# Optimization experiments

Hardware: AMD Instinct MI355X
Metric: run time of the kernel (lower is better)

Reference implementation:

```python
import jax, jax.numpy as jnp
import numpy as np

C = 256; NH = 8; HD = C // NH; NL = 4; NP = 4; DFF = 1024
B = 8; NQ = 900
SHAPES = ((100, 100), (50, 50), (25, 25), (13, 13))
LEN = sum(h * w for h, w in SHAPES)


def setup_inputs() -> dict:
    key = jax.random.key(0)
    ks = jax.random.split(key, 16)
    s = 0.02
    d = {}
    d['tgt'] = jax.random.normal(ks[0], (B, NQ, C), jnp.float32)
    d['query_pos'] = jax.random.normal(ks[1], (B, NQ, C), jnp.float32)
    d['reference_points'] = jax.random.uniform(ks[2], (B, NQ, NL, 2), jnp.float32)
    d['src'] = jax.random.normal(ks[3], (B, LEN, C), jnp.float32)
    d['spatial_shapes'] = np.array(SHAPES, dtype=np.int32)
    # self-attn (nn.MultiheadAttention) params, stored [in,out]
    d['sa_in_w'] = jax.random.normal(ks[4], (C, 3 * C), jnp.float32) * s
    d['sa_in_b'] = jnp.zeros((3 * C,), jnp.float32)
    d['sa_out_w'] = jax.random.normal(ks[5], (C, C), jnp.float32) * s
    d['sa_out_b'] = jnp.zeros((C,), jnp.float32)
    d['ln2_g'] = jnp.ones((C,), jnp.float32); d['ln2_b'] = jnp.zeros((C,), jnp.float32)
    # MSDeformAttn params
    d['off_w'] = jax.random.normal(ks[6], (C, NH * NL * NP * 2), jnp.float32) * s
    d['off_b'] = jax.random.normal(ks[7], (NH * NL * NP * 2,), jnp.float32) * 0.5
    d['attw_w'] = jax.random.normal(ks[8], (C, NH * NL * NP), jnp.float32) * s
    d['attw_b'] = jnp.zeros((NH * NL * NP,), jnp.float32)
    d['val_w'] = jax.random.normal(ks[9], (C, C), jnp.float32) * s
    d['val_b'] = jnp.zeros((C,), jnp.float32)
    d['proj_w'] = jax.random.normal(ks[10], (C, C), jnp.float32) * s
    d['proj_b'] = jnp.zeros((C,), jnp.float32)
    d['ln1_g'] = jnp.ones((C,), jnp.float32); d['ln1_b'] = jnp.zeros((C,), jnp.float32)
    # FFN
    d['lin1_w'] = jax.random.normal(ks[11], (C, DFF), jnp.float32) * s
    d['lin1_b'] = jnp.zeros((DFF,), jnp.float32)
    d['lin2_w'] = jax.random.normal(ks[12], (DFF, C), jnp.float32) * s
    d['lin2_b'] = jnp.zeros((C,), jnp.float32)
    d['ln3_g'] = jnp.ones((C,), jnp.float32); d['ln3_b'] = jnp.zeros((C,), jnp.float32)
    return d


def _ln(x, g, b):
    m = jnp.mean(x, -1, keepdims=True)
    v = jnp.mean((x - m) ** 2, -1, keepdims=True)
    return (x - m) * jax.lax.rsqrt(v + 1e-5) * g + b


def _bilinear(v, loc, H, W):
    # v: [B,NH,H*W,HD]; loc: [B,NQ,NH,NP,2] normalized to [0,1]
    # matches F.grid_sample(align_corners=False, padding_mode='zeros')
    b = v.shape[0]; nq = loc.shape[1]
    x = loc[..., 0] * W - 0.5
    y = loc[..., 1] * H - 0.5
    x0 = jnp.floor(x); y0 = jnp.floor(y)
    dx = x - x0; dy = y - y0
    x0i = x0.astype(jnp.int32); y0i = y0.astype(jnp.int32)

    def gat(ix, iy):
        valid = ((ix >= 0) & (ix < W) & (iy >= 0) & (iy < H)).astype(v.dtype)
        idx = jnp.clip(iy, 0, H - 1) * W + jnp.clip(ix, 0, W - 1)  # [B,NQ,NH,NP]
        idx_t = jnp.transpose(idx, (0, 2, 1, 3)).reshape(b, NH, nq * NP)
        g = jnp.take_along_axis(v, idx_t[..., None], axis=2).reshape(b, NH, nq, NP, HD)
        return g * jnp.transpose(valid, (0, 2, 1, 3))[..., None]

    wt = lambda a: jnp.transpose(a, (0, 2, 1, 3))[..., None]
    return (gat(x0i, y0i) * wt((1 - dx) * (1 - dy))
            + gat(x0i + 1, y0i) * wt(dx * (1 - dy))
            + gat(x0i, y0i + 1) * wt((1 - dx) * dy)
            + gat(x0i + 1, y0i + 1) * wt(dx * dy))


def _msda(q, ref, src, shapes, val_w, val_b, off_w, off_b, attw_w, attw_b, proj_w, proj_b):
    b, nq, _ = q.shape
    value = jnp.transpose((src @ val_w + val_b).reshape(b, -1, NH, HD), (0, 2, 1, 3))  # [B,NH,Len,HD]
    off = (q @ off_w + off_b).reshape(b, nq, NH, NL, NP, 2)
    aw = jax.nn.softmax((q @ attw_w + attw_b).reshape(b, nq, NH, NL * NP), -1)
    aw = aw.reshape(b, nq, NH, NL, NP)
    acc = jnp.zeros((b, NH, nq, HD), q.dtype)
    start = 0
    for l, (H_, W_) in enumerate(shapes):
        norm = jnp.array([W_, H_], q.dtype)
        loc = ref[:, :, None, l, None, :] + off[:, :, :, l] / norm  # [B,NQ,NH,NP,2]
        smp = _bilinear(value[:, :, start:start + H_ * W_], loc, H_, W_)  # [B,NH,NQ,NP,HD]
        acc = acc + jnp.sum(smp * jnp.transpose(aw[:, :, :, l], (0, 2, 1, 3))[..., None], axis=3)
        start += H_ * W_
    out = jnp.transpose(acc, (0, 2, 1, 3)).reshape(b, nq, C)
    return out @ proj_w + proj_b


def _self_attn(x, pos, in_w, in_b, out_w, out_b):
    b, nq, _ = x.shape
    qk = x + pos
    q = (qk @ in_w[:, :C] + in_b[:C]).reshape(b, nq, NH, HD)
    k = (qk @ in_w[:, C:2 * C] + in_b[C:2 * C]).reshape(b, nq, NH, HD)
    v = (x @ in_w[:, 2 * C:] + in_b[2 * C:]).reshape(b, nq, NH, HD)
    att = jax.nn.softmax(jnp.einsum('bqhd,bkhd->bhqk', q, k) * (1.0 / float(np.sqrt(HD))), -1)
    o = jnp.einsum('bhqk,bkhd->bqhd', att, v).reshape(b, nq, C)
    return o @ out_w + out_b


def _forward(tgt, query_pos, reference_points, src, shapes,
             sa_in_w, sa_in_b, sa_out_w, sa_out_b, ln2_g, ln2_b,
             off_w, off_b, attw_w, attw_b, val_w, val_b, proj_w, proj_b, ln1_g, ln1_b,
             lin1_w, lin1_b, lin2_w, lin2_b, ln3_g, ln3_b):
    t2 = _self_attn(tgt, query_pos, sa_in_w, sa_in_b, sa_out_w, sa_out_b)
    t = _ln(tgt + t2, ln2_g, ln2_b)
    t2 = _msda(t + query_pos, reference_points, src, shapes,
               val_w, val_b, off_w, off_b, attw_w, attw_b, proj_w, proj_b)
    t = _ln(t + t2, ln1_g, ln1_b)
    h = jax.nn.relu(t @ lin1_w + lin1_b) @ lin2_w + lin2_b
    return _ln(t + h, ln3_g, ln3_b)


def reference(tgt, query_pos, reference_points, src, spatial_shapes,
              sa_in_w, sa_in_b, sa_out_w, sa_out_b, ln2_g, ln2_b,
              off_w, off_b, attw_w, attw_b, val_w, val_b, proj_w, proj_b, ln1_g, ln1_b,
              lin1_w, lin1_b, lin2_w, lin2_b, ln3_g, ln3_b):
    shapes = [(int(h), int(w)) for h, w in np.asarray(spatial_shapes)]
    return _forward(tgt, query_pos, reference_points, src, shapes,
                    sa_in_w, sa_in_b, sa_out_w, sa_out_b, ln2_g, ln2_b,
                    off_w, off_b, attw_w, attw_b, val_w, val_b, proj_w, proj_b, ln1_g, ln1_b,
                    lin1_w, lin1_b, lin2_w, lin2_b, ln3_g, ln3_b)
```

## Files before the change

### kernel.cpp

```cpp
#include <hip/hip_runtime.h>
#include <hip/hip_bf16.h>
#include <type_traits>

#define C_DIM 256
#define NHEAD 8
#define HDIM 32
#define NLVL 4
#define NPT 4
#define DFF_DIM 1024
#define BB 8
#define NQ_DIM 900
#define LEN_DIM 13294
#define ROWS (BB * NQ_DIM)
#define VROWS (BB * LEN_DIM)

typedef __attribute__((ext_vector_type(8))) short short8v;
typedef __attribute__((ext_vector_type(8))) unsigned short ushort8v;
typedef __attribute__((ext_vector_type(4))) float float4v;
typedef __attribute__((ext_vector_type(4))) unsigned short ushort4v;

__device__ __forceinline__ float bf2f(unsigned short u) {
  union { unsigned int i; float f; } v; v.i = ((unsigned int)u) << 16; return v.f;
}
__device__ __forceinline__ unsigned short f2bf(float f) {
  __hip_bfloat16 h = __float2bfloat16(f);
  return *reinterpret_cast<unsigned short*>(&h);
}

__global__ __launch_bounds__(256) void wconv_kernel(
    const float* __restrict__ w0, const float* __restrict__ w1,
    const float* __restrict__ w2, const float* __restrict__ w3,
    const float* __restrict__ w4, const float* __restrict__ w5,
    const float* __restrict__ w6, const float* __restrict__ w7,
    unsigned short* __restrict__ out) {
  const int Ks[8] = {256, 256, 256, 256, 256, 256, 256, 1024};
  const int Ns[8] = {768, 256, 256, 128, 256, 256, 1024, 256};
  const int Oo[8] = {0, 196608, 262144, 327680, 360448, 425984, 491520, 753664};
  int w = blockIdx.y;
  int K = Ks[w], N = Ns[w];
  int ntx = N >> 5, nty = K >> 5;
  if ((int)blockIdx.x >= ntx * nty) return;
  int tx = blockIdx.x % ntx, ty = blockIdx.x / ntx;
  const float* W = w == 0 ? w0 : w == 1 ? w1 : w == 2 ? w2 : w == 3 ? w3
                 : w == 4 ? w4 : w == 5 ? w5 : w == 6 ? w6 : w7;
  __shared__ float tile[32][33];
  int c = threadIdx.x & 31, rg = threadIdx.x >> 5;
#pragma unroll
  for (int j = 0; j < 4; ++j) {
    int k = ty * 32 + rg * 4 + j;
    tile[rg * 4 + j][c] = W[(size_t)k * N + tx * 32 + c];
  }
  __syncthreads();
  unsigned short* o = out + Oo[w];
#pragma unroll
  for (int j = 0; j < 4; ++j) {
    int n = tx * 32 + rg * 4 + j;
    o[(size_t)n * K + ty * 32 + c] = f2bf(tile[c][rg * 4 + j]);
  }
}

__global__ __launch_bounds__(256) void prep_kernel(const float* __restrict__ a,
                                                   const float* __restrict__ b,
                                                   unsigned short* __restrict__ o1,
                                                   unsigned short* __restrict__ o2, int n4) {
  int i = blockIdx.x * 256 + threadIdx.x;
  if (i < n4) {
    float4 x = reinterpret_cast<const float4*>(a)[i];
    float4 y = reinterpret_cast<const float4*>(b)[i];
    ushort4v u1, u2;
    u1[0] = f2bf(x.x); u1[1] = f2bf(x.y); u1[2] = f2bf(x.z); u1[3] = f2bf(x.w);
    u2[0] = f2bf(x.x + y.x); u2[1] = f2bf(x.y + y.y);
    u2[2] = f2bf(x.z + y.z); u2[3] = f2bf(x.w + y.w);
    *reinterpret_cast<ushort4v*>(o1 + (size_t)i * 4) = u1;
    *reinterpret_cast<ushort4v*>(o2 + (size_t)i * 4) = u2;
  }
}

template <typename TA, typename TO, int RELU>
__device__ __forceinline__ void gemm_body(
    unsigned short* smem,
    const TA* __restrict__ A, const TA* __restrict__ A2,
    const unsigned short* __restrict__ Wt,
    const float* __restrict__ bias, const float* __restrict__ bias2,
    TO* __restrict__ Cout, TO* __restrict__ Cout2,
    int M, int N, int K, int lda, int ldc, int ldc2, int colSplit,
    int bx, int by) {
  auto Al = reinterpret_cast<unsigned short(*)[128][40]>(smem);
  auto Wl = reinterpret_cast<unsigned short(*)[128][40]>(smem + 10240);
  const int tid = threadIdx.x;
  const int lane = tid & 63, wid = tid >> 6;
  const int g = lane >> 4, ql = lane & 15;
  const int wr = wid >> 1, wc = wid & 1;
  const int row0 = by * 128, col0 = bx * 128;

  const TA* Ause = (A2 != nullptr && col0 >= colSplit) ? A2 : A;

  float4v acc[4][4];
#pragma unroll
  for (int i = 0; i < 4; ++i)
#pragma unroll
    for (int j = 0; j < 4; ++j) acc[i][j] = (float4v){0.f, 0.f, 0.f, 0.f};

  float4 areg_f[4];
  ushort8v areg_b[2];
  ushort8v wreg[2];

  auto loadA = [&](int k0) {
    if constexpr (std::is_same<TA, float>::value) {
#pragma unroll
      for (int j = 0; j < 4; ++j) {
        int c = tid + 256 * j;
        int row = c >> 3, f4 = c & 7;
        int gr = min(row0 + row, M - 1);
        areg_f[j] = *reinterpret_cast<const float4*>(Ause + (size_t)gr * lda + k0 + f4 * 4);
      }
    } else {
#pragma unroll
      for (int j = 0; j < 2; ++j) {
        int c = tid + 256 * j;
        int row = c >> 2, ch = c & 3;
        int gr = min(row0 + row, M - 1);
        areg_b[j] = *reinterpret_cast<const ushort8v*>(
            reinterpret_cast<const unsigned short*>(Ause) + (size_t)gr * lda + k0 + ch * 8);
      }
    }
  };
  auto loadW = [&](int k0) {
#pragma unroll
    for (int j = 0; j < 2; ++j) {
      int c = tid + 256 * j;
      int row = c >> 2, ch = c & 3;
      wreg[j] = *reinterpret_cast<const ushort8v*>(
          Wt + (size_t)(col0 + row) * K + k0 + ch * 8);
    }
  };
  auto storeA = [&](int buf) {
    if constexpr (std::is_same<TA, float>::value) {
#pragma unroll
      for (int j = 0; j < 4; ++j) {
        int c = tid + 256 * j;
        int row = c >> 3, f4 = c & 7;
        ushort4v u;
        u[0] = f2bf(areg_f[j].x); u[1] = f2bf(areg_f[j].y);
        u[2] = f2bf(areg_f[j].z); u[3] = f2bf(areg_f[j].w);
        *reinterpret_cast<ushort4v*>(&Al[buf][row][f4 * 4]) = u;
      }
    } else {
#pragma unroll
      for (int j = 0; j < 2; ++j) {
        int c = tid + 256 * j;
        int row = c >> 2, ch = c & 3;
        *reinterpret_cast<ushort8v*>(&Al[buf][row][ch * 8]) = areg_b[j];
      }
    }
  };
  auto storeW = [&](int buf) {
#pragma unroll
    for (int j = 0; j < 2; ++j) {
      int c = tid + 256 * j;
      int row = c >> 2, ch = c & 3;
      *reinterpret_cast<ushort8v*>(&Wl[buf][row][ch * 8]) = wreg[j];
    }
  };

  const int nt = K >> 5;
  loadA(0); loadW(0);
  storeA(0); storeW(0);

  for (int t = 0; t < nt; ++t) {
    __syncthreads();
    if (t + 1 < nt) { loadA((t + 1) << 5); loadW((t + 1) << 5); }
    const int cur = t & 1;
    short8v af[4], bfr[4];
#pragma unroll
    for (int mi = 0; mi < 4; ++mi)
      af[mi] = *reinterpret_cast<const short8v*>(&Al[cur][wr * 64 + mi * 16 + ql][8 * g]);
#pragma unroll
    for (int ni = 0; ni < 4; ++ni)
      bfr[ni] = *reinterpret_cast<const short8v*>(&Wl[cur][wc * 64 + ni * 16 + ql][8 * g]);
#pragma unroll
    for (int mi = 0; mi < 4; ++mi)
#pragma unroll
      for (int ni = 0; ni < 4; ++ni)
        acc[mi][ni] = __builtin_amdgcn_mfma_f32_16x16x32_bf16(af[mi], bfr[ni], acc[mi][ni], 0, 0, 0);
    if (t + 1 < nt) { storeA(cur ^ 1); storeW(cur ^ 1); }
  }

  const bool sel2 = (Cout2 != nullptr && col0 >= colSplit);
  const float* bsrc = sel2 ? bias2 : bias;
  TO* outp = sel2 ? Cout2 : Cout;
  const int ldco = sel2 ? ldc2 : ldc;
  const int cbase = sel2 ? (col0 - colSplit) : col0;
  float bv[4];
#pragma unroll
  for (int ni = 0; ni < 4; ++ni) bv[ni] = bsrc[cbase + wc * 64 + ni * 16 + ql];
#pragma unroll
  for (int mi = 0; mi < 4; ++mi) {
#pragma unroll
    for (int r = 0; r < 4; ++r) {
      int row = row0 + wr * 64 + mi * 16 + 4 * g + r;
      if (row >= M) continue;
#pragma unroll
      for (int ni = 0; ni < 4; ++ni) {
        int col = cbase + wc * 64 + ni * 16 + ql;
        float v = acc[mi][ni][r] + bv[ni];
        if (RELU) v = fmaxf(v, 0.f);
        if constexpr (std::is_same<TO, float>::value) {
          outp[(size_t)row * ldco + col] = v;
        } else {
          outp[(size_t)row * ldco + col] = __float2bfloat16(v);
        }
      }
    }
  }
}

template <typename TA, typename TO, int RELU>
__global__ __launch_bounds__(256) void mfma_gemm_kernel(
    const TA* __restrict__ A, const TA* __restrict__ A2,
    const unsigned short* __restrict__ Wt,
    const float* __restrict__ bias, const float* __restrict__ bias2,
    TO* __restrict__ Cout, TO* __restrict__ Cout2,
    int M, int N, int K, int lda, int ldc, int ldc2, int colSplit) {
  __shared__ unsigned short smem[20480];
  gemm_body<TA, TO, RELU>(smem, A, A2, Wt, bias, bias2, Cout, Cout2,
                          M, N, K, lda, ldc, ldc2, colSplit,
                          blockIdx.x, blockIdx.y);
}

#define QKV_BLOCKS (6 * 57)
__global__ __launch_bounds__(256) void qkv_value_kernel(
    const unsigned short* __restrict__ x0bf, const unsigned short* __restrict__ tgtbf,
    const unsigned short* __restrict__ sa_inT, const float* __restrict__ sa_in_b,
    __hip_bfloat16* __restrict__ qkv,
    const float* __restrict__ src, const unsigned short* __restrict__ valT,
    const float* __restrict__ val_b, __hip_bfloat16* __restrict__ value) {
  __shared__ unsigned short smem[20480];
  int bid = blockIdx.x;
  if (bid < QKV_BLOCKS) {
    gemm_body<unsigned short, __hip_bfloat16, 0>(
        smem, x0bf, tgtbf, sa_inT, sa_in_b, nullptr, qkv, nullptr,
        ROWS, 768, 256, 256, 768, 0, 512, bid % 6, bid / 6);
  } else {
    int t = bid - QKV_BLOCKS;
    gemm_body<float, __hip_bfloat16, 0>(
        smem, src, nullptr, valT, val_b, nullptr, value, nullptr,
        VROWS, 256, 256, 256, 256, 0, 1 << 30, t & 1, t >> 1);
  }
}

__global__ __launch_bounds__(256) void ln_fused_kernel(const float* __restrict__ x,
                                                       const float* __restrict__ y,
                                                       const float* __restrict__ gg,
                                                       const float* __restrict__ bb,
                                                       float* __restrict__ out,
                                                       unsigned short* __restrict__ out2,
                                                       const float* __restrict__ qadd) {
  int row = blockIdx.x, t = threadIdx.x;
  size_t base = (size_t)row * C_DIM + t;
  float v = x[base] + y[base];
  float s = v, s2 = v * v;
#pragma unroll
  for (int o = 32; o > 0; o >>= 1) {
    s += __shfl_xor(s, o);
    s2 += __shfl_xor(s2, o);
  }
  __shared__ float w1[4], w2[4];
  int wid = t >> 6, lane = t & 63;
  if (lane == 0) { w1[wid] = s; w2[wid] = s2; }
  __syncthreads();
  float S = w1[0] + w1[1] + w1[2] + w1[3];
  float S2 = w2[0] + w2[1] + w2[2] + w2[3];
  float mean = S * (1.f / 256.f);
  float var = S2 * (1.f / 256.f) - mean * mean;
  float rstd = rsqrtf(var + 1e-5f);
  float r = (v - mean) * rstd * gg[t] + bb[t];
  out[base] = r;
  if (out2) {
    float r2 = qadd ? (r + qadd[base]) : r;
    out2[base] = f2bf(r2);
  }
}

__global__ __launch_bounds__(256) void self_attn_mfma_kernel(
    const unsigned short* __restrict__ qkv, unsigned short* __restrict__ out) {
  __shared__ unsigned short V_lds[2][32][16];
  __shared__ unsigned short P_lds[4][16][32];
  const int tid = threadIdx.x;
  const int lane = tid & 63, wid = tid >> 6;
  const int g = lane >> 4, ql = lane & 15;
  const int bh = blockIdx.y;
  const int b = bh >> 3, h = bh & 7;
  const int q0 = blockIdx.x * 64 + wid * 16;
  const float scale = 0.17677669529663687f;

  const unsigned short* qkv_b = qkv + (size_t)b * NQ_DIM * 768;
  const int qrow = min(q0 + ql, NQ_DIM - 1);
  short8v qf = *reinterpret_cast<const short8v*>(
      qkv_b + (size_t)qrow * 768 + h * HDIM + 8 * g);

  float4v o0 = {0.f, 0.f, 0.f, 0.f}, o1 = {0.f, 0.f, 0.f, 0.f};
  float m = -1e30f, lsum = 0.f;

  const int sk = tid >> 3;
  const int sd = (tid & 7) * 4;
  const int sdb = sd >> 4, sdi = sd & 15;

  const int NT = 29;
  for (int kt = 0; kt < NT; ++kt) {
    __syncthreads();
    {
      int kg = min(kt * 32 + sk, NQ_DIM - 1);
      ushort4v v4 = *reinterpret_cast<const ushort4v*>(
          qkv_b + (size_t)kg * 768 + 512 + h * HDIM + sd);
      *reinterpret_cast<ushort4v*>(&V_lds[sdb][sk][sdi]) = v4;
    }
    __syncthreads();

    const int k_base = kt * 32;
    int kr0 = min(k_base + ql, NQ_DIM - 1);
    int kr1 = min(k_base + 16 + ql, NQ_DIM - 1);
    short8v kf0 = *reinterpret_cast<const short8v*>(
        qkv_b + (size_t)kr0 * 768 + 256 + h * HDIM + 8 * g);
    short8v kf1 = *reinterpret_cast<const short8v*>(
        qkv_b + (size_t)kr1 * 768 + 256 + h * HDIM + 8 * g);
    float4v z = {0.f, 0.f, 0.f, 0.f};
    float4v s0 = __builtin_amdgcn_mfma_f32_16x16x32_bf16(kf0, qf, z, 0, 0, 0);
    float4v s1 = __builtin_amdgcn_mfma_f32_16x16x32_bf16(kf1, qf, z, 0, 0, 0);

    float s[8];
#pragma unroll
    for (int r = 0; r < 4; ++r) { s[r] = s0[r] * scale; s[4 + r] = s1[r] * scale; }
    if (kt == NT - 1) {
#pragma unroll
      for (int i = 0; i < 8; ++i) {
        int kk = k_base + 16 * (i >> 2) + 4 * g + (i & 3);
        if (kk >= NQ_DIM) s[i] = -1e30f;
      }
    }
    float tm = s[0];
#pragma unroll
    for (int i = 1; i < 8; ++i) tm = fmaxf(tm, s[i]);
    tm = fmaxf(tm, __shfl_xor(tm, 16));
    tm = fmaxf(tm, __shfl_xor(tm, 32));
    float mnew = fmaxf(m, tm);
    float alpha = __expf(m - mnew);
    float p[8];
    float ts = 0.f;
#pragma unroll
    for (int i = 0; i < 8; ++i) { p[i] = __expf(s[i] - mnew); ts += p[i]; }
    ts += __shfl_xor(ts, 16);
    ts += __shfl_xor(ts, 32);
    lsum = lsum * alpha + ts;
    m = mnew;

    ushort4v pp0, pp1;
#pragma unroll
    for (int r = 0; r < 4; ++r) { pp0[r] = f2bf(p[r]); pp1[r] = f2bf(p[4 + r]); }
    *reinterpret_cast<ushort4v*>(&P_lds[wid][ql][4 * g]) = pp0;
    *reinterpret_cast<ushort4v*>(&P_lds[wid][ql][16 + 4 * g]) = pp1;
    asm volatile("s_waitcnt lgkmcnt(0)" ::: "memory");
    __builtin_amdgcn_sched_barrier(0);

    o0 *= alpha;
    o1 *= alpha;

    short8v pf = *reinterpret_cast<const short8v*>(&P_lds[wid][ql][8 * g]);
    short8v vf0, vf1;
#pragma unroll
    for (int i = 0; i < 8; ++i) {
      vf0[i] = (short)V_lds[0][8 * g + i][ql];
      vf1[i] = (short)V_lds[1][8 * g + i][ql];
    }
    o0 = __builtin_amdgcn_mfma_f32_16x16x32_bf16(vf0, pf, o0, 0, 0, 0);
    o1 = __builtin_amdgcn_mfma_f32_16x16x32_bf16(vf1, pf, o1, 0, 0, 0);
  }

  float inv = 1.f / lsum;
  if (q0 + ql < NQ_DIM) {
    unsigned short* op = out + ((size_t)(b * NQ_DIM) + q0 + ql) * C_DIM + h * HDIM;
    ushort4v u0, u1;
#pragma unroll
    for (int r = 0; r < 4; ++r) { u0[r] = f2bf(o0[r] * inv); u1[r] = f2bf(o1[r] * inv); }
    *reinterpret_cast<ushort4v*>(op + 4 * g) = u0;
    *reinterpret_cast<ushort4v*>(op + 16 + 4 * g) = u1;
  }
}

__global__ __launch_bounds__(256) void softmax16_kernel(float* __restrict__ aw, int total) {
  int t = blockIdx.x * 256 + threadIdx.x;
  if (t >= total) return;
  float* p = aw + (size_t)t * 16;
  float vals[16];
  float m = -1e30f;
#pragma unroll
  for (int i = 0; i < 16; ++i) { vals[i] = p[i]; m = fmaxf(m, vals[i]); }
  float s = 0.f;
#pragma unroll
  for (int i = 0; i < 16; ++i) { vals[i] = __expf(vals[i] - m); s += vals[i]; }
  float inv = 1.f / s;
#pragma unroll
  for (int i = 0; i < 16; ++i) p[i] = vals[i] * inv;
}

__global__ __launch_bounds__(256) void msda_sample_kernel(
    const unsigned short* __restrict__ value,
    const float* __restrict__ off,
    const float* __restrict__ aw,
    const float* __restrict__ refp,
    const int* __restrict__ shapes,
    unsigned short* __restrict__ out) {
  int g = blockIdx.x * 32 + (threadIdx.x >> 3);
  int d4 = threadIdx.x & 7;
  int h = g & 7;
  int row = g >> 3;
  int b = row / NQ_DIM;
  float acc0 = 0.f, acc1 = 0.f, acc2 = 0.f, acc3 = 0.f;
  int start = 0;
  const float* offr = off + (size_t)row * 256 + h * 32;
  const float* awr  = aw + (size_t)row * 128 + h * 16;
  const float* rpr  = refp + (size_t)row * NLVL * 2;
#pragma unroll
  for (int l = 0; l < NLVL; ++l) {
    int Hl = shapes[2 * l], Wl = shapes[2 * l + 1];
    float fx = rpr[2 * l + 0] * (float)Wl - 0.5f;
    float fy = rpr[2 * l + 1] * (float)Hl - 0.5f;
    const unsigned short* vbase =
        value + ((size_t)(b * LEN_DIM + start)) * C_DIM + h * HDIM + d4 * 4;
#pragma unroll
    for (int p = 0; p < NPT; ++p) {
      float x = fx + offr[l * 8 + p * 2];
      float y = fy + offr[l * 8 + p * 2 + 1];
      float a = awr[l * 4 + p];
      float x0f = floorf(x), y0f = floorf(y);
      float dx = x - x0f, dy = y - y0f;
      int x0 = (int)x0f, y0 = (int)y0f;
      int x1 = x0 + 1, y1 = y0 + 1;
      float wx1 = dx, wx0 = 1.f - dx;
      float wy1 = dy * a, wy0 = (1.f - dy) * a;
      bool vx0 = ((unsigned)x0 < (unsigned)Wl);
      bool vx1 = ((unsigned)x1 < (unsigned)Wl);
      bool vy0 = ((unsigned)y0 < (unsigned)Hl);
      bool vy1 = ((unsigned)y1 < (unsigned)Hl);
      float w00 = (vx0 && vy0) ? wx0 * wy0 : 0.f;
      float w10 = (vx1 && vy0) ? wx1 * wy0 : 0.f;
      float w01 = (vx0 && vy1) ? wx0 * wy1 : 0.f;
      float w11 = (vx1 && vy1) ? wx1 * wy1 : 0.f;
      int x0c = min(max(x0, 0), Wl - 1), x1c = min(max(x1, 0), Wl - 1);
      int y0c = min(max(y0, 0), Hl - 1), y1c = min(max(y1, 0), Hl - 1);
      int r0 = y0c * Wl, r1 = y1c * Wl;
      ushort4v g00 = *reinterpret_cast<const ushort4v*>(vbase + ((r0 + x0c) << 8));
      ushort4v g10 = *reinterpret_cast<const ushort4v*>(vbase + ((r0 + x1c) << 8));
      ushort4v g01 = *reinterpret_cast<const ushort4v*>(vbase + ((r1 + x0c) << 8));
      ushort4v g11 = *reinterpret_cast<const ushort4v*>(vbase + ((r1 + x1c) << 8));
      acc0 += w00 * bf2f(g00[0]) + w10 * bf2f(g10[0]) + w01 * bf2f(g01[0]) + w11 * bf2f(g11[0]);
      acc1 += w00 * bf2f(g00[1]) + w10 * bf2f(g10[1]) + w01 * bf2f(g01[1]) + w11 * bf2f(g11[1]);
      acc2 += w00 * bf2f(g00[2]) + w10 * bf2f(g10[2]) + w01 * bf2f(g01[2]) + w11 * bf2f(g11[2]);
      acc3 += w00 * bf2f(g00[3]) + w10 * bf2f(g10[3]) + w01 * bf2f(g01[3]) + w11 * bf2f(g11[3]);
    }
    start += Hl * Wl;
  }
  ushort4v o;
  o[0] = f2bf(acc0); o[1] = f2bf(acc1); o[2] = f2bf(acc2); o[3] = f2bf(acc3);
  *reinterpret_cast<ushort4v*>(out + (size_t)row * C_DIM + h * HDIM + d4 * 4) = o;
}

extern "C" void kernel_launch(void* const* d_in, const int* in_sizes, int n_in,
                              void* d_out, int out_size, void* d_ws, size_t ws_size,
                              hipStream_t stream) {
  const float* tgt      = (const float*)d_in[0];
  const float* qpos     = (const float*)d_in[1];
  const float* refp     = (const float*)d_in[2];
  const float* src      = (const float*)d_in[3];
  const int*   shapes   = (const int*)d_in[4];
  const float* sa_in_w  = (const float*)d_in[5];
  const float* sa_in_b  = (const float*)d_in[6];
  const float* sa_out_w = (const float*)d_in[7];
  const float* sa_out_b = (const float*)d_in[8];
  const float* ln2_g    = (const float*)d_in[9];
  const float* ln2_b    = (const float*)d_in[10];
  const float* off_w    = (const float*)d_in[11];
  const float* off_b    = (const float*)d_in[12];
  const float* attw_w   = (const float*)d_in[13];
  const float* attw_b   = (const float*)d_in[14];
  const float* val_w    = (const float*)d_in[15];
  const float* val_b    = (const float*)d_in[16];
  const float* proj_w   = (const float*)d_in[17];
  const float* proj_b   = (const float*)d_in[18];
  const float* ln1_g    = (const float*)d_in[19];
  const float* ln1_b    = (const float*)d_in[20];
  const float* lin1_w   = (const float*)d_in[21];
  const float* lin1_b   = (const float*)d_in[22];
  const float* lin2_w   = (const float*)d_in[23];
  const float* lin2_b   = (const float*)d_in[24];
  const float* ln3_g    = (const float*)d_in[25];
  const float* ln3_b    = (const float*)d_in[26];

  char* ws = (char*)d_ws;
  size_t off_b_ws = 0;
  auto alloc = [&](size_t bytes) {
    char* p = ws + off_b_ws;
    off_b_ws += (bytes + 255) & ~(size_t)255;
    return p;
  };
  unsigned short* wT     = (unsigned short*)alloc((size_t)1015808 * 2);
  unsigned short* value  = (unsigned short*)alloc((size_t)VROWS * C_DIM * 2);
  unsigned short* qkvh   = (unsigned short*)alloc((size_t)ROWS * 768 * 2);
  unsigned short* tgtbf  = (unsigned short*)alloc((size_t)ROWS * C_DIM * 2);
  unsigned short* X0bf   = (unsigned short*)alloc((size_t)ROWS * C_DIM * 2);
  unsigned short* attnbf = (unsigned short*)alloc((size_t)ROWS * C_DIM * 2);
  unsigned short* X3bf   = (unsigned short*)alloc((size_t)ROWS * C_DIM * 2);
  unsigned short* sampbf = (unsigned short*)alloc((size_t)ROWS * C_DIM * 2);
  unsigned short* X6bf   = (unsigned short*)alloc((size_t)ROWS * C_DIM * 2);
  unsigned short* hidbf  = (unsigned short*)alloc((size_t)ROWS * DFF_DIM * 2);
  float* X1 = (float*)alloc((size_t)ROWS * C_DIM * 4);
  float* X2 = (float*)alloc((size_t)ROWS * C_DIM * 4);
  float* X4 = (float*)alloc((size_t)ROWS * C_DIM * 4);
  float* X5 = (float*)alloc((size_t)ROWS * 128 * 4);
  float* X6 = (float*)alloc((size_t)ROWS * C_DIM * 4);
  if (off_b_ws > ws_size) return;

  unsigned short* sa_inT = wT + 0;
  unsigned short* sa_outT = wT + 196608;
  unsigned short* offT   = wT + 262144;
  unsigned short* valT   = wT + 360448;
  unsigned short* projT  = wT + 425984;
  unsigned short* lin1T  = wT + 491520;
  unsigned short* lin2T  = wT + 753664;

  dim3 blk(256);
  const int MB7200 = (ROWS + 127) / 128;
  const int MBV = (VROWS + 127) / 128;
  int n4 = ROWS * C_DIM / 4;
  int addBlocks = (n4 + 255) / 256;

  wconv_kernel<<<dim3(256, 8), blk, 0, stream>>>(
      sa_in_w, sa_out_w, off_w, attw_w, val_w, proj_w, lin1_w, lin2_w, wT);
  prep_kernel<<<addBlocks, blk, 0, stream>>>(tgt, qpos, tgtbf, X0bf, n4);

  qkv_value_kernel<<<QKV_BLOCKS + 2 * MBV, blk, 0, stream>>>(
      X0bf, tgtbf, sa_inT, sa_in_b, (__hip_bfloat16*)qkvh,
      src, valT, val_b, (__hip_bfloat16*)value);

  self_attn_mfma_kernel<<<dim3(15, 64), blk, 0, stream>>>(qkvh, attnbf);
  mfma_gemm_kernel<unsigned short, float, 0><<<dim3(2, MB7200), blk, 0, stream>>>(
      attnbf, nullptr, sa_outT, sa_out_b, nullptr,
      X1, nullptr, ROWS, 256, 256, 256, 256, 0, 1 << 30);
  ln_fused_kernel<<<ROWS, blk, 0, stream>>>(tgt, X1, ln2_g, ln2_b, X2, X3bf, qpos);

  mfma_gemm_kernel<unsigned short, float, 0><<<dim3(3, MB7200), blk, 0, stream>>>(
      X3bf, nullptr, offT, off_b, attw_b,
      X4, X5, ROWS, 384, 256, 256, 256, 128, 256);
  softmax16_kernel<<<(ROWS * NHEAD + 255) / 256, blk, 0, stream>>>(X5, ROWS * NHEAD);
  msda_sample_kernel<<<ROWS * NHEAD / 32, blk, 0, stream>>>(
      value, X4, X5, refp, shapes, sampbf);
  mfma_gemm_kernel<unsigned short, float, 0><<<dim3(2, MB7200), blk, 0, stream>>>(
      sampbf, nullptr, projT, proj_b, nullptr,
      X1, nullptr, ROWS, 256, 256, 256, 256, 0, 1 << 30);
  ln_fused_kernel<<<ROWS, blk, 0, stream>>>(X2, X1, ln1_g, ln1_b, X6, X6bf, nullptr);

  mfma_gemm_kernel<unsigned short, __hip_bfloat16, 1><<<dim3(8, MB7200), blk, 0, stream>>>(
      X6bf, nullptr, lin1T, lin1_b, nullptr,
      (__hip_bfloat16*)hidbf, nullptr, ROWS, 1024, 256, 256, 1024, 0, 1 << 30);
  mfma_gemm_kernel<unsigned short, float, 0><<<dim3(2, MB7200), blk, 0, stream>>>(
      hidbf, nullptr, lin2T, lin2_b, nullptr,
      X1, nullptr, ROWS, 256, 1024, 1024, 256, 0, 1 << 30);
  ln_fused_kernel<<<ROWS, blk, 0, stream>>>(X6, X1, ln3_g, ln3_b, (float*)d_out, nullptr, nullptr);
}
```

Baseline: 230.8 us.

## Write V transposed from QKV GEMM epilogue and drop LDS V staging in self-attention

The QKV projection epilogue now writes Q and K to a 512-wide buffer and V to a per-batch transposed [C][928] buffer. The self-attention kernel can then load V fragments straight from global memory as contiguous short8 vectors. This removes the per-tile LDS staging, the scalar transpose gather and two __syncthreads per key tile. The weight-conversion and input-prep kernels are also merged into one launch to save launch overhead. In exchange, the transposed epilogue uses strided 2-byte global stores. The padded key columns 900..927 of the V buffer are never written, so garbage there (for example NaN) could leak into the output even though those keys get zero probability.

Measured after the change: 231.9 us. About the same (+0.5%).

```diff
diff --git a/kernel.cpp b/kernel.cpp
--- a/kernel.cpp
+++ b/kernel.cpp
@@ -13,6 +13,7 @@
 #define LEN_DIM 13294
 #define ROWS (BB * NQ_DIM)
 #define VROWS (BB * LEN_DIM)
+#define VT_LD 928
 
 typedef __attribute__((ext_vector_type(8))) short short8v;
 typedef __attribute__((ext_vector_type(8))) unsigned short ushort8v;
@@ -27,56 +28,57 @@
   return *reinterpret_cast<unsigned short*>(&h);
 }
 
-__global__ __launch_bounds__(256) void wconv_kernel(
+#define WCONV_BLOCKS 2048
+__global__ __launch_bounds__(256) void wprep_kernel(
     const float* __restrict__ w0, const float* __restrict__ w1,
     const float* __restrict__ w2, const float* __restrict__ w3,
     const float* __restrict__ w4, const float* __restrict__ w5,
     const float* __restrict__ w6, const float* __restrict__ w7,
-    unsigned short* __restrict__ out) {
-  const int Ks[8] = {256, 256, 256, 256, 256, 256, 256, 1024};
-  const int Ns[8] = {768, 256, 256, 128, 256, 256, 1024, 256};
-  const int Oo[8] = {0, 196608, 262144, 327680, 360448, 425984, 491520, 753664};
-  int w = blockIdx.y;
-  int K = Ks[w], N = Ns[w];
-  int ntx = N >> 5, nty = K >> 5;
-  if ((int)blockIdx.x >= ntx * nty) return;
-  int tx = blockIdx.x % ntx, ty = blockIdx.x / ntx;
-  const float* W = w == 0 ? w0 : w == 1 ? w1 : w == 2 ? w2 : w == 3 ? w3
-                 : w == 4 ? w4 : w == 5 ? w5 : w == 6 ? w6 : w7;
-  __shared__ float tile[32][33];
-  int c = threadIdx.x & 31, rg = threadIdx.x >> 5;
-#pragma unroll
-  for (int j = 0; j < 4; ++j) {
-    int k = ty * 32 + rg * 4 + j;
-    tile[rg * 4 + j][c] = W[(size_t)k * N + tx * 32 + c];
-  }
-  __syncthreads();
-  unsigned short* o = out + Oo[w];
-#pragma unroll
-  for (int j = 0; j < 4; ++j) {
-    int n = tx * 32 + rg * 4 + j;
-    o[(size_t)n * K + ty * 32 + c] = f2bf(tile[c][rg * 4 + j]);
-  }
-}
-
-__global__ __launch_bounds__(256) void prep_kernel(const float* __restrict__ a,
-                                                   const float* __restrict__ b,
-                                                   unsigned short* __restrict__ o1,
-                                                   unsigned short* __restrict__ o2, int n4) {
-  int i = blockIdx.x * 256 + threadIdx.x;
-  if (i < n4) {
-    float4 x = reinterpret_cast<const float4*>(a)[i];
-    float4 y = reinterpret_cast<const float4*>(b)[i];
-    ushort4v u1, u2;
-    u1[0] = f2bf(x.x); u1[1] = f2bf(x.y); u1[2] = f2bf(x.z); u1[3] = f2bf(x.w);
-    u2[0] = f2bf(x.x + y.x); u2[1] = f2bf(x.y + y.y);
-    u2[2] = f2bf(x.z + y.z); u2[3] = f2bf(x.w + y.w);
-    *reinterpret_cast<ushort4v*>(o1 + (size_t)i * 4) = u1;
-    *reinterpret_cast<ushort4v*>(o2 + (size_t)i * 4) = u2;
-  }
-}
-
-template <typename TA, typename TO, int RELU>
+    unsigned short* __restrict__ out,
+    const float* __restrict__ tgt, const float* __restrict__ qpos,
+    unsigned short* __restrict__ tgtbf, unsigned short* __restrict__ x0bf, int n4) {
+  int bid = blockIdx.x;
+  if (bid < WCONV_BLOCKS) {
+    const int Ks[8] = {256, 256, 256, 256, 256, 256, 256, 1024};
+    const int Ns[8] = {768, 256, 256, 128, 256, 256, 1024, 256};
+    const int Oo[8] = {0, 196608, 262144, 327680, 360448, 425984, 491520, 753664};
+    int w = bid >> 8, bx = bid & 255;
+    int K = Ks[w], N = Ns[w];
+    int ntx = N >> 5, nty = K >> 5;
+    if (bx >= ntx * nty) return;
+    int tx = bx % ntx, ty = bx / ntx;
+    const float* W = w == 0 ? w0 : w == 1 ? w1 : w == 2 ? w2 : w == 3 ? w3
+                   : w == 4 ? w4 : w == 5 ? w5 : w == 6 ? w6 : w7;
+    __shared__ float tile[32][33];
+    int c = threadIdx.x & 31, rg = threadIdx.x >> 5;
+#pragma unroll
+    for (int j = 0; j < 4; ++j) {
+      int k = ty * 32 + rg * 4 + j;
+      tile[rg * 4 + j][c] = W[(size_t)k * N + tx * 32 + c];
+    }
+    __syncthreads();
+    unsigned short* o = out + Oo[w];
+#pragma unroll
+    for (int j = 0; j < 4; ++j) {
+      int n = tx * 32 + rg * 4 + j;
+      o[(size_t)n * K + ty * 32 + c] = f2bf(tile[c][rg * 4 + j]);
+    }
+  } else {
+    int i = (bid - WCONV_BLOCKS) * 256 + threadIdx.x;
+    if (i < n4) {
+      float4 x = reinterpret_cast<const float4*>(tgt)[i];
+      float4 y = reinterpret_cast<const float4*>(qpos)[i];
+      ushort4v u1, u2;
+      u1[0] = f2bf(x.x); u1[1] = f2bf(x.y); u1[2] = f2bf(x.z); u1[3] = f2bf(x.w);
+      u2[0] = f2bf(x.x + y.x); u2[1] = f2bf(x.y + y.y);
+      u2[2] = f2bf(x.z + y.z); u2[3] = f2bf(x.w + y.w);
+      *reinterpret_cast<ushort4v*>(tgtbf + (size_t)i * 4) = u1;
+      *reinterpret_cast<ushort4v*>(x0bf + (size_t)i * 4) = u2;
+    }
+  }
+}
+
+template <typename TA, typename TO, int RELU, int VT>
 __device__ __forceinline__ void gemm_body(
     unsigned short* smem,
     const TA* __restrict__ A, const TA* __restrict__ A2,
@@ -187,10 +189,31 @@
   }
 
   const bool sel2 = (Cout2 != nullptr && col0 >= colSplit);
+  const int cbase = sel2 ? (col0 - colSplit) : col0;
+  if (VT && sel2) {
+    unsigned short* vTp = reinterpret_cast<unsigned short*>(Cout2);
+    float bv[4];
+#pragma unroll
+    for (int ni = 0; ni < 4; ++ni) bv[ni] = bias2[cbase + wc * 64 + ni * 16 + ql];
+#pragma unroll
+    for (int mi = 0; mi < 4; ++mi) {
+#pragma unroll
+      for (int r = 0; r < 4; ++r) {
+        int row = row0 + wr * 64 + mi * 16 + 4 * g + r;
+        if (row >= M) continue;
+        int bb = row / 900, rr = row - bb * 900;
+#pragma unroll
+        for (int ni = 0; ni < 4; ++ni) {
+          int c = cbase + wc * 64 + ni * 16 + ql;
+          vTp[((size_t)bb * 256 + c) * VT_LD + rr] = f2bf(acc[mi][ni][r] + bv[ni]);
+        }
+      }
+    }
+    return;
+  }
   const float* bsrc = sel2 ? bias2 : bias;
   TO* outp = sel2 ? Cout2 : Cout;
   const int ldco = sel2 ? ldc2 : ldc;
-  const int cbase = sel2 ? (col0 - colSplit) : col0;
   float bv[4];
 #pragma unroll
   for (int ni = 0; ni < 4; ++ni) bv[ni] = bsrc[cbase + wc * 64 + ni * 16 + ql];
@@ -223,27 +246,27 @@
     TO* __restrict__ Cout, TO* __restrict__ Cout2,
     int M, int N, int K, int lda, int ldc, int ldc2, int colSplit) {
   __shared__ unsigned short smem[20480];
-  gemm_body<TA, TO, RELU>(smem, A, A2, Wt, bias, bias2, Cout, Cout2,
-                          M, N, K, lda, ldc, ldc2, colSplit,
-                          blockIdx.x, blockIdx.y);
+  gemm_body<TA, TO, RELU, 0>(smem, A, A2, Wt, bias, bias2, Cout, Cout2,
+                             M, N, K, lda, ldc, ldc2, colSplit,
+                             blockIdx.x, blockIdx.y);
 }
 
 #define QKV_BLOCKS (6 * 57)
 __global__ __launch_bounds__(256) void qkv_value_kernel(
     const unsigned short* __restrict__ x0bf, const unsigned short* __restrict__ tgtbf,
     const unsigned short* __restrict__ sa_inT, const float* __restrict__ sa_in_b,
-    __hip_bfloat16* __restrict__ qkv,
+    __hip_bfloat16* __restrict__ qkbuf, __hip_bfloat16* __restrict__ vT,
     const float* __restrict__ src, const unsigned short* __restrict__ valT,
     const float* __restrict__ val_b, __hip_bfloat16* __restrict__ value) {
   __shared__ unsigned short smem[20480];
   int bid = blockIdx.x;
   if (bid < QKV_BLOCKS) {
-    gemm_body<unsigned short, __hip_bfloat16, 0>(
-        smem, x0bf, tgtbf, sa_inT, sa_in_b, nullptr, qkv, nullptr,
-        ROWS, 768, 256, 256, 768, 0, 512, bid % 6, bid / 6);
+    gemm_body<unsigned short, __hip_bfloat16, 0, 1>(
+        smem, x0bf, tgtbf, sa_inT, sa_in_b, sa_in_b + 512, qkbuf, vT,
+        ROWS, 768, 256, 256, 512, 0, 512, bid % 6, bid / 6);
   } else {
     int t = bid - QKV_BLOCKS;
-    gemm_body<float, __hip_bfloat16, 0>(
+    gemm_body<float, __hip_bfloat16, 0, 0>(
         smem, src, nullptr, valT, val_b, nullptr, value, nullptr,
         VROWS, 256, 256, 256, 256, 0, 1 << 30, t & 1, t >> 1);
   }
@@ -283,8 +306,8 @@
 }
 
 __global__ __launch_bounds__(256) void self_attn_mfma_kernel(
-    const unsigned short* __restrict__ qkv, unsigned short* __restrict__ out) {
-  __shared__ unsigned short V_lds[2][32][16];
+    const unsigned short* __restrict__ qk, const unsigned short* __restrict__ vT,
+    unsigned short* __restrict__ out) {
   __shared__ unsigned short P_lds[4][16][32];
   const int tid = threadIdx.x;
   const int lane = tid & 63, wid = tid >> 6;
@@ -294,36 +317,24 @@
   const int q0 = blockIdx.x * 64 + wid * 16;
   const float scale = 0.17677669529663687f;
 
-  const unsigned short* qkv_b = qkv + (size_t)b * NQ_DIM * 768;
+  const unsigned short* qk_b = qk + (size_t)b * NQ_DIM * 512;
   const int qrow = min(q0 + ql, NQ_DIM - 1);
   short8v qf = *reinterpret_cast<const short8v*>(
-      qkv_b + (size_t)qrow * 768 + h * HDIM + 8 * g);
+      qk_b + (size_t)qrow * 512 + h * HDIM + 8 * g);
+  const unsigned short* kb = qk_b + 256 + h * HDIM + 8 * g;
+  const unsigned short* vtb0 = vT + ((size_t)b * 256 + h * HDIM + ql) * VT_LD;
+  const unsigned short* vtb1 = vtb0 + 16 * VT_LD;
 
   float4v o0 = {0.f, 0.f, 0.f, 0.f}, o1 = {0.f, 0.f, 0.f, 0.f};
   float m = -1e30f, lsum = 0.f;
 
-  const int sk = tid >> 3;
-  const int sd = (tid & 7) * 4;
-  const int sdb = sd >> 4, sdi = sd & 15;
-
   const int NT = 29;
   for (int kt = 0; kt < NT; ++kt) {
-    __syncthreads();
-    {
-      int kg = min(kt * 32 + sk, NQ_DIM - 1);
-      ushort4v v4 = *reinterpret_cast<const ushort4v*>(
-          qkv_b + (size_t)kg * 768 + 512 + h * HDIM + sd);
-      *reinterpret_cast<ushort4v*>(&V_lds[sdb][sk][sdi]) = v4;
-    }
-    __syncthreads();
-
     const int k_base = kt * 32;
     int kr0 = min(k_base + ql, NQ_DIM - 1);
     int kr1 = min(k_base + 16 + ql, NQ_DIM - 1);
-    short8v kf0 = *reinterpret_cast<const short8v*>(
-        qkv_b + (size_t)kr0 * 768 + 256 + h * HDIM + 8 * g);
-    short8v kf1 = *reinterpret_cast<const short8v*>(
-        qkv_b + (size_t)kr1 * 768 + 256 + h * HDIM + 8 * g);
+    short8v kf0 = *reinterpret_cast<const short8v*>(kb + (size_t)kr0 * 512);
+    short8v kf1 = *reinterpret_cast<const short8v*>(kb + (size_t)kr1 * 512);
     float4v z = {0.f, 0.f, 0.f, 0.f};
     float4v s0 = __builtin_amdgcn_mfma_f32_16x16x32_bf16(kf0, qf, z, 0, 0, 0);
     float4v s1 = __builtin_amdgcn_mfma_f32_16x16x32_bf16(kf1, qf, z, 0, 0, 0);
@@ -366,12 +377,8 @@
     o1 *= alpha;
 
     short8v pf = *reinterpret_cast<const short8v*>(&P_lds[wid][ql][8 * g]);
-    short8v vf0, vf1;
-#pragma unroll
-    for (int i = 0; i < 8; ++i) {
-      vf0[i] = (short)V_lds[0][8 * g + i][ql];
-      vf1[i] = (short)V_lds[1][8 * g + i][ql];
-    }
+    short8v vf0 = *reinterpret_cast<const short8v*>(vtb0 + k_base + 8 * g);
+    short8v vf1 = *reinterpret_cast<const short8v*>(vtb1 + k_base + 8 * g);
     o0 = __builtin_amdgcn_mfma_f32_16x16x32_bf16(vf0, pf, o0, 0, 0, 0);
     o1 = __builtin_amdgcn_mfma_f32_16x16x32_bf16(vf1, pf, o1, 0, 0, 0);
   }
@@ -505,7 +512,8 @@
   };
   unsigned short* wT     = (unsigned short*)alloc((size_t)1015808 * 2);
   unsigned short* value  = (unsigned short*)alloc((size_t)VROWS * C_DIM * 2);
-  unsigned short* qkvh   = (unsigned short*)alloc((size_t)ROWS * 768 * 2);
+  unsigned short* qkbuf  = (unsigned short*)alloc((size_t)ROWS * 512 * 2);
+  unsigned short* vTbuf  = (unsigned short*)alloc((size_t)BB * 256 * VT_LD * 2);
   unsigned short* tgtbf  = (unsigned short*)alloc((size_t)ROWS * C_DIM * 2);
   unsigned short* X0bf   = (unsigned short*)alloc((size_t)ROWS * C_DIM * 2);
   unsigned short* attnbf = (unsigned short*)alloc((size_t)ROWS * C_DIM * 2);
@@ -532,17 +540,17 @@
   const int MB7200 = (ROWS + 127) / 128;
   const int MBV = (VROWS + 127) / 128;
   int n4 = ROWS * C_DIM / 4;
-  int addBlocks = (n4 + 255) / 256;
-
-  wconv_kernel<<<dim3(256, 8), blk, 0, stream>>>(
-      sa_in_w, sa_out_w, off_w, attw_w, val_w, proj_w, lin1_w, lin2_w, wT);
-  prep_kernel<<<addBlocks, blk, 0, stream>>>(tgt, qpos, tgtbf, X0bf, n4);
+  int prepBlocks = (n4 + 255) / 256;
+
+  wprep_kernel<<<WCONV_BLOCKS + prepBlocks, blk, 0, stream>>>(
+      sa_in_w, sa_out_w, off_w, attw_w, val_w, proj_w, lin1_w, lin2_w, wT,
+      tgt, qpos, tgtbf, X0bf, n4);
 
   qkv_value_kernel<<<QKV_BLOCKS + 2 * MBV, blk, 0, stream>>>(
-      X0bf, tgtbf, sa_inT, sa_in_b, (__hip_bfloat16*)qkvh,
+      X0bf, tgtbf, sa_inT, sa_in_b, (__hip_bfloat16*)qkbuf, (__hip_bfloat16*)vTbuf,
       src, valT, val_b, (__hip_bfloat16*)value);
 
-  self_attn_mfma_kernel<<<dim3(15, 64), blk, 0, stream>>>(qkvh, attnbf);
+  self_attn_mfma_kernel<<<dim3(15, 64), blk, 0, stream>>>(qkbuf, vTbuf, attnbf);
   mfma_gemm_kernel<unsigned short, float, 0><<<dim3(2, MB7200), blk, 0, stream>>>(
       attnbf, nullptr, sa_outT, sa_out_b, nullptr,
       X1, nullptr, ROWS, 256, 256, 256, 256, 0, 1 << 30);
```
